# Kernel optimization log

Measured on AMD Instinct MI355X. Metric: run time of the kernel, lower is better.

The kernel has to match this reference:

```python
import jax, jax.numpy as jnp
import numpy as np
from jax import lax

NUM_CHANNELS = 64
DILATION_DEPTH = 9
NUM_REPEAT = 2
KERNEL_SIZE = 3
DILATIONS = [2 ** d for d in range(DILATION_DEPTH)] * NUM_REPEAT  # 18 layers
B, T = 4, 32768


def causal_conv1d(x, w, b, dilation):
    # x: [B, Cin, T], w: [Cout, Cin, K], b: [Cout]
    # left-pad by (K-1)*dilation -> causal, output length T
    pad = (w.shape[-1] - 1) * dilation
    out = lax.conv_general_dilated(
        x, w, window_strides=(1,), padding=[(pad, 0)],
        rhs_dilation=(dilation,), dimension_numbers=("NCH", "OIH", "NCH"))
    return out + b[None, :, None]


def setup_inputs() -> dict:
    key = jax.random.key(0)
    ks = jax.random.split(key, 9)
    L, C = len(DILATIONS), NUM_CHANNELS
    s = 0.05
    return {
        "x": jax.random.normal(ks[0], (B, 1, T), dtype=jnp.float32),
        "in_w": jax.random.normal(ks[1], (C, 1, 1), dtype=jnp.float32) * s,
        "in_b": jax.random.normal(ks[2], (C,), dtype=jnp.float32) * s,
        "hid_w": jax.random.normal(ks[3], (L, 2 * C, C, KERNEL_SIZE), dtype=jnp.float32) * s,
        "hid_b": jax.random.normal(ks[4], (L, 2 * C), dtype=jnp.float32) * s,
        "res_w": jax.random.normal(ks[5], (L, C, C, 1), dtype=jnp.float32) * s,
        "res_b": jax.random.normal(ks[6], (L, C), dtype=jnp.float32) * s,
        "mix_w": jax.random.normal(ks[7], (1, L * C, 1), dtype=jnp.float32) * s,
        "mix_b": jax.random.normal(ks[8], (1,), dtype=jnp.float32) * s,
    }


def reference(x, in_w, in_b, hid_w, hid_b, res_w, res_b, mix_w, mix_b):
    C = NUM_CHANNELS
    out = causal_conv1d(x, in_w, in_b, 1)  # [B, C, T]
    skips = []
    for i, d in enumerate(DILATIONS):
        inp = out
        h = causal_conv1d(inp, hid_w[i], hid_b[i], d)  # [B, 2C, T]
        gated = jnp.tanh(h[:, :C]) * jax.nn.sigmoid(h[:, C:])  # [B, C, T]
        skips.append(gated)
        out = causal_conv1d(gated, res_w[i], res_b[i], 1) + inp
    skip_cat = jnp.concatenate(skips, axis=1)  # [B, L*C, T]
    return causal_conv1d(skip_cat, mix_w, mix_b, 1)  # [B, 1, T]
```

## Files before the change

kernel.cpp:

```cpp
#include <hip/hip_runtime.h>
#include <math.h>

#define T_LEN 32768
#define NB 4
#define NC 64
#define NL 18
#define TILE_T 64

typedef __attribute__((ext_vector_type(8))) short s16x8;
typedef __attribute__((ext_vector_type(4))) float f32x4;
#define MFMA_F16 __builtin_amdgcn_mfma_f32_16x16x32_f16

__device__ inline unsigned short f2h(float f) {
    _Float16 h = (_Float16)f;
    return __builtin_bit_cast(unsigned short, h);
}
__device__ inline unsigned pack_h2(float a, float b) {
    return (unsigned)f2h(a) | ((unsigned)f2h(b) << 16);
}
__device__ inline float h2f(unsigned short u) {
    return (float)__builtin_bit_cast(_Float16, u);
}
__device__ inline float fast_sigmoid(float x) {
    return __builtin_amdgcn_rcpf(1.f + __expf(-x));
}
__device__ inline float fast_tanh(float x) {
    return 1.f - 2.f * __builtin_amdgcn_rcpf(1.f + __expf(2.f * x));
}

__global__ void prep_kernel(const float* __restrict__ hid_w,
                            const float* __restrict__ res_w,
                            const float* __restrict__ mix_b,
                            unsigned short* __restrict__ Wh,
                            unsigned short* __restrict__ Wr,
                            float* __restrict__ out,
                            float* __restrict__ zerobuf) {
    const int nW1 = NL * 128 * 192;
    const int nW2 = NL * 64 * 64;
    const int nOut = NB * T_LEN;
    const int total = nW1 + nW2 + nOut + 32;
    for (int gid = blockIdx.x * blockDim.x + threadIdx.x; gid < total;
         gid += gridDim.x * blockDim.x) {
        if (gid < nW1) {
            int K = gid % 192;
            int co = (gid / 192) & 127;
            int i = gid / (192 * 128);
            int kt = K >> 6, ci = K & 63;
            Wh[gid] = f2h(hid_w[((i * 128 + co) * 64 + ci) * 3 + kt]);
        } else if (gid < nW1 + nW2) {
            int q = gid - nW1;
            int c = q & 63, co = (q >> 6) & 63, i = q >> 12;
            Wr[q] = f2h(res_w[(i * 64 + co) * 64 + c]);
        } else if (gid < nW1 + nW2 + nOut) {
            out[gid - (nW1 + nW2)] = mix_b[0];
        } else {
            zerobuf[gid - (nW1 + nW2 + nOut)] = 0.f;
        }
    }
}

template <int DIL, bool FIRST, bool LAST>
__launch_bounds__(256, 4)
__global__ void layer_kernel(const unsigned short* __restrict__ actH,
                             unsigned short* __restrict__ outH,
                             const unsigned short* __restrict__ Wh,
                             const float* __restrict__ hb,
                             const unsigned short* __restrict__ Wr,
                             const float* __restrict__ rb,
                             const float* __restrict__ mw,
                             float* __restrict__ skip,
                             const float* __restrict__ zerobuf,
                             const float* __restrict__ x,
                             const float* __restrict__ in_w,
                             const float* __restrict__ in_b) {
    constexpr bool UNI = (DIL < 64);
    constexpr int R = UNI ? (64 + 2 * DIL) : 192;
    constexpr int SLOTS = R * 8;
    constexpr int JMAX = (SLOTS + 255) / 256;
    constexpr int GS_BASE = (UNI ? 128 : 0) * 128;
    constexpr int OUT_BASE = (UNI ? 0 : 64) * 128;

    __shared__ uint4 Xs[1536];
    __shared__ float Sk[256];
    char* lds = (char*)Xs;

    const int tid = threadIdx.x;
    const int w = tid >> 6;
    const int l = tid & 63;
    const int lo = l & 15;
    const int hi = l >> 4;
    const int b = blockIdx.y;
    const int tile = (blockIdx.x & 7) * 64 + (blockIdx.x >> 3);
    const int t0 = tile * TILE_T;
    const int m0 = 16 * w;
    const int c0 = m0 + 4 * hi;

    const unsigned short* actB = actH + (size_t)b * T_LEN * NC;
    const float* xB = x + (size_t)b * T_LEN;

    if (FIRST) {
#pragma unroll
        for (int j = 0; j < JMAX; j++) {
            int p = j * 256 + tid;
            if (p < SLOTS) {
                int row = p >> 3, ch = p & 7;
                int tg = t0 + row - 2 * DIL;
                unsigned uu[4] = {0u, 0u, 0u, 0u};
                if (tg >= 0) {
                    float a = xB[tg];
#pragma unroll
                    for (int e = 0; e < 4; e++) {
                        float v0 = a * in_w[ch * 8 + 2 * e] + in_b[ch * 8 + 2 * e];
                        float v1 = a * in_w[ch * 8 + 2 * e + 1] + in_b[ch * 8 + 2 * e + 1];
                        uu[e] = pack_h2(v0, v1);
                    }
                }
                int byte = (row * 128 + ch * 16) ^ ((row & 7) << 4);
                *(uint4*)(lds + byte) = make_uint4(uu[0], uu[1], uu[2], uu[3]);
            }
        }
    } else {
#pragma unroll
        for (int j = 0; j < JMAX; j++) {
            int s = (w * JMAX + j) * 64 + l;
            const void* src;
            if (s >= SLOTS) {
                src = (const void*)(zerobuf + (s & 7) * 4);
            } else {
                int row = s >> 3, ch = s & 7;
                int chunk = ch ^ (row & 7);
                int tg = t0 + (UNI ? (row - 2 * DIL)
                                   : (((row >> 6) - 2) * DIL + (row & 63)));
                src = (tg >= 0) ? (const void*)(actB + (size_t)tg * 64 + chunk * 8)
                                : (const void*)(zerobuf + chunk * 4);
            }
            __builtin_amdgcn_global_load_lds(
                (const __attribute__((address_space(1))) unsigned int*)src,
                (__attribute__((address_space(3))) unsigned int*)(lds +
                                                        (w * JMAX + j) * 1024),
                16, 0, 0);
        }
    }

    s16x8 AH[2][6];
    s16x8 AR[2];
#pragma unroll
    for (int mt = 0; mt < 2; mt++) {
        const unsigned short* wp = Wh + (size_t)(m0 + 64 * mt + lo) * 192;
#pragma unroll
        for (int s = 0; s < 6; s++)
            AH[mt][s] = *(const s16x8*)(wp + 32 * s + 8 * hi);
    }
    if (!LAST) {
#pragma unroll
        for (int s = 0; s < 2; s++)
            AR[s] = *(const s16x8*)(Wr + (size_t)(m0 + lo) * 64 + 32 * s + 8 * hi);
    }

    float bA[4], bB[4], rbv[4];
#pragma unroll
    for (int r = 0; r < 4; r++) {
        bA[r] = hb[c0 + r];
        bB[r] = hb[64 + c0 + r];
        rbv[r] = LAST ? 0.f : rb[c0 + r];
    }
    const float4 mw4 = *(const float4*)(mw + c0);

    __syncthreads();

    f32x4 acc[2][4];
#pragma unroll
    for (int mt = 0; mt < 2; mt++)
#pragma unroll
        for (int nt = 0; nt < 4; nt++)
            acc[mt][nt] = (f32x4){0.f, 0.f, 0.f, 0.f};

#pragma unroll
    for (int s = 0; s < 6; s++) {
        const int tap = s >> 1, half = s & 1;
#pragma unroll
        for (int nt = 0; nt < 4; nt++) {
            int t = 16 * nt + lo;
            int row = UNI ? (t + tap * DIL) : (tap * 64 + t);
            int byte = (row * 128 + half * 64 + hi * 16) ^ ((row & 7) << 4);
            s16x8 bx = __builtin_bit_cast(s16x8, *(const uint4*)(lds + byte));
            acc[0][nt] = MFMA_F16(AH[0][s], bx, acc[0][nt], 0, 0, 0);
            acc[1][nt] = MFMA_F16(AH[1][s], bx, acc[1][nt], 0, 0, 0);
        }
    }

    float4 inp[4];
    if (!LAST) {
#pragma unroll
        for (int nt = 0; nt < 4; nt++) {
            int t = 16 * nt + lo;
            int rowI = UNI ? (t + 2 * DIL) : (128 + t);
            int byteI = (rowI * 128 + c0 * 2) ^ ((rowI & 7) << 4);
            uint2 hv = *(const uint2*)(lds + byteI);
            inp[nt] = make_float4(h2f((unsigned short)(hv.x & 0xffff)),
                                  h2f((unsigned short)(hv.x >> 16)),
                                  h2f((unsigned short)(hv.y & 0xffff)),
                                  h2f((unsigned short)(hv.y >> 16)));
        }
    }

    __syncthreads();

#pragma unroll
    for (int nt = 0; nt < 4; nt++) {
        float g[4];
#pragma unroll
        for (int r = 0; r < 4; r++) {
            float hA = acc[0][nt][r] + bA[r];
            float hB = acc[1][nt][r] + bB[r];
            g[r] = fast_tanh(hA) * fast_sigmoid(hB);
        }
        int t = 16 * nt + lo;
        if (!LAST) {
            int byte = (t * 128 + c0 * 2) ^ ((t & 7) << 4);
            *(uint2*)(lds + GS_BASE + byte) =
                make_uint2(pack_h2(g[0], g[1]), pack_h2(g[2], g[3]));
        }
        float sk = g[0] * mw4.x + g[1] * mw4.y + g[2] * mw4.z + g[3] * mw4.w;
        sk += __shfl_xor(sk, 16, 64);
        sk += __shfl_xor(sk, 32, 64);
        if (hi == 0) Sk[w * 64 + nt * 16 + lo] = sk;
    }
    __syncthreads();

    if (LAST) {
        if (tid < 64) {
            float s2 = Sk[tid] + Sk[64 + tid] + Sk[128 + tid] + Sk[192 + tid];
            skip[(size_t)b * T_LEN + t0 + tid] += s2;
        }
        return;
    }

    f32x4 acc2[4];
#pragma unroll
    for (int nt = 0; nt < 4; nt++) acc2[nt] = (f32x4){0.f, 0.f, 0.f, 0.f};
#pragma unroll
    for (int s = 0; s < 2; s++) {
#pragma unroll
        for (int nt = 0; nt < 4; nt++) {
            int t = 16 * nt + lo;
            int byte = (t * 128 + s * 64 + hi * 16) ^ ((t & 7) << 4);
            s16x8 bg = __builtin_bit_cast(
                s16x8, *(const uint4*)(lds + GS_BASE + byte));
            acc2[nt] = MFMA_F16(AR[s], bg, acc2[nt], 0, 0, 0);
        }
    }

    char* OutH = lds + OUT_BASE;
#pragma unroll
    for (int nt = 0; nt < 4; nt++) {
        int t = 16 * nt + lo;
        float ox = acc2[nt][0] + rbv[0] + inp[nt].x;
        float oy = acc2[nt][1] + rbv[1] + inp[nt].y;
        float oz = acc2[nt][2] + rbv[2] + inp[nt].z;
        float ow = acc2[nt][3] + rbv[3] + inp[nt].w;
        int byteB = (t * 128 + c0 * 2) ^ ((t & 7) << 4);
        *(uint2*)(OutH + byteB) = make_uint2(pack_h2(ox, oy), pack_h2(oz, ow));
    }

    if (tid < 64) {
        float s2 = Sk[tid] + Sk[64 + tid] + Sk[128 + tid] + Sk[192 + tid];
        skip[(size_t)b * T_LEN + t0 + tid] += s2;
    }
    __syncthreads();

    unsigned short* gH = outH + (size_t)b * T_LEN * NC + (size_t)t0 * 64;
#pragma unroll
    for (int i = 0; i < 2; i++) {
        int u = i * 256 + tid;
        int t = u >> 3, ch = u & 7;
        uint4 v = *(const uint4*)(OutH + t * 128 + ((ch ^ (t & 7)) << 4));
        ((uint4*)gH)[u] = v;
    }
}

extern "C" void kernel_launch(void* const* d_in, const int* in_sizes, int n_in,
                              void* d_out, int out_size, void* d_ws, size_t ws_size,
                              hipStream_t stream) {
    const float* x     = (const float*)d_in[0];
    const float* in_w  = (const float*)d_in[1];
    const float* in_b  = (const float*)d_in[2];
    const float* hid_w = (const float*)d_in[3];
    const float* hid_b = (const float*)d_in[4];
    const float* res_w = (const float*)d_in[5];
    const float* res_b = (const float*)d_in[6];
    const float* mix_w = (const float*)d_in[7];
    const float* mix_b = (const float*)d_in[8];
    float* out = (float*)d_out;

    const size_t actN = (size_t)NB * T_LEN * NC;
    unsigned short* H0 = (unsigned short*)d_ws;
    unsigned short* H1 = H0 + actN;
    unsigned short* Wh = H1 + actN;
    unsigned short* Wr = Wh + (size_t)NL * 128 * 192;
    float* zerobuf = (float*)(Wr + (size_t)NL * 64 * 64);

    prep_kernel<<<512, 256, 0, stream>>>(hid_w, res_w, mix_b, Wh, Wr, out,
                                         zerobuf);

    static const int dils[NL] = {1, 2, 4, 8, 16, 32, 64, 128, 256,
                                 1, 2, 4, 8, 16, 32, 64, 128, 256};
    const unsigned short* srcH = H0;
    unsigned short* dstH = H1;
    dim3 grid(T_LEN / TILE_T, NB);

#define LL(D, F, L)                                                           \
    layer_kernel<D, F, L><<<grid, 256, 0, stream>>>(                          \
        srcH, dstH, Wh + (size_t)i * 128 * 192, hid_b + (size_t)i * 128,      \
        Wr + (size_t)i * 64 * 64, res_b + (size_t)i * 64,                     \
        mix_w + (size_t)i * 64, out, zerobuf, x, in_w, in_b)

    for (int i = 0; i < NL; i++) {
        if (i == 0) {
            LL(1, true, false);
        } else if (i == NL - 1) {
            LL(256, false, true);
        } else {
            switch (dils[i]) {
                case 1:   LL(1, false, false);   break;
                case 2:   LL(2, false, false);   break;
                case 4:   LL(4, false, false);   break;
                case 8:   LL(8, false, false);   break;
                case 16:  LL(16, false, false);  break;
                case 32:  LL(32, false, false);  break;
                case 64:  LL(64, false, false);  break;
                case 128: LL(128, false, false); break;
                case 256: LL(256, false, false); break;
            }
        }
        const unsigned short* tH = srcH; srcH = dstH; dstH = (unsigned short*)tH;
    }
#undef LL
}
```

Before: 380.2 us.

## Process two 64-step subtiles per block with double-buffered async LDS loads

Each block now handles 128 time steps as two 64-step subtiles, issuing the global-to-LDS loads for both subtiles up front into separate LDS regions. Barriers wait only on the first subtile's loads (vmcnt(JMAX)), so the second subtile's loads can overlap the first subtile's MFMA and gating work. It also halves the grid and amortizes per-block weight and bias register loads across two subtiles. LDS use doubles per block, which may reduce occupancy, and the custom waitcnt barriers depend on the load-issue order staying as written.

```diff
diff --git a/kernel.cpp b/kernel.cpp
--- a/kernel.cpp
+++ b/kernel.cpp
@@ -5,11 +5,24 @@
 #define NB 4
 #define NC 64
 #define NL 18
-#define TILE_T 64
 
 typedef __attribute__((ext_vector_type(8))) short s16x8;
 typedef __attribute__((ext_vector_type(4))) float f32x4;
 #define MFMA_F16 __builtin_amdgcn_mfma_f32_16x16x32_f16
+
+#define BAR_LGKM()                                                   \
+    do {                                                             \
+        asm volatile("s_waitcnt lgkmcnt(0)" ::: "memory");           \
+        __builtin_amdgcn_s_barrier();                                \
+        __builtin_amdgcn_sched_barrier(0);                           \
+    } while (0)
+#define BAR_VM(N)                                                    \
+    do {                                                             \
+        asm volatile("s_waitcnt vmcnt(%0) lgkmcnt(0)" ::             \
+                         "i"(N) : "memory");                         \
+        __builtin_amdgcn_s_barrier();                                \
+        __builtin_amdgcn_sched_barrier(0);                           \
+    } while (0)
 
 __device__ inline unsigned short f2h(float f) {
     _Float16 h = (_Float16)f;
@@ -79,8 +92,9 @@
     constexpr int JMAX = (SLOTS + 255) / 256;
     constexpr int GS_BASE = (UNI ? 128 : 0) * 128;
     constexpr int OUT_BASE = (UNI ? 0 : 64) * 128;
-
-    __shared__ uint4 Xs[1536];
+    constexpr int REG = 24576;
+
+    __shared__ uint4 Xs[2 * 1536];
     __shared__ float Sk[256];
     char* lds = (char*)Xs;
 
@@ -90,58 +104,14 @@
     const int lo = l & 15;
     const int hi = l >> 4;
     const int b = blockIdx.y;
-    const int tile = (blockIdx.x & 7) * 64 + (blockIdx.x >> 3);
-    const int t0 = tile * TILE_T;
+    const int tile = (blockIdx.x & 7) * 32 + (blockIdx.x >> 3);
+    const int t0 = tile * 128;
     const int m0 = 16 * w;
     const int c0 = m0 + 4 * hi;
 
     const unsigned short* actB = actH + (size_t)b * T_LEN * NC;
     const float* xB = x + (size_t)b * T_LEN;
 
-    if (FIRST) {
-#pragma unroll
-        for (int j = 0; j < JMAX; j++) {
-            int p = j * 256 + tid;
-            if (p < SLOTS) {
-                int row = p >> 3, ch = p & 7;
-                int tg = t0 + row - 2 * DIL;
-                unsigned uu[4] = {0u, 0u, 0u, 0u};
-                if (tg >= 0) {
-                    float a = xB[tg];
-#pragma unroll
-                    for (int e = 0; e < 4; e++) {
-                        float v0 = a * in_w[ch * 8 + 2 * e] + in_b[ch * 8 + 2 * e];
-                        float v1 = a * in_w[ch * 8 + 2 * e + 1] + in_b[ch * 8 + 2 * e + 1];
-                        uu[e] = pack_h2(v0, v1);
-                    }
-                }
-                int byte = (row * 128 + ch * 16) ^ ((row & 7) << 4);
-                *(uint4*)(lds + byte) = make_uint4(uu[0], uu[1], uu[2], uu[3]);
-            }
-        }
-    } else {
-#pragma unroll
-        for (int j = 0; j < JMAX; j++) {
-            int s = (w * JMAX + j) * 64 + l;
-            const void* src;
-            if (s >= SLOTS) {
-                src = (const void*)(zerobuf + (s & 7) * 4);
-            } else {
-                int row = s >> 3, ch = s & 7;
-                int chunk = ch ^ (row & 7);
-                int tg = t0 + (UNI ? (row - 2 * DIL)
-                                   : (((row >> 6) - 2) * DIL + (row & 63)));
-                src = (tg >= 0) ? (const void*)(actB + (size_t)tg * 64 + chunk * 8)
-                                : (const void*)(zerobuf + chunk * 4);
-            }
-            __builtin_amdgcn_global_load_lds(
-                (const __attribute__((address_space(1))) unsigned int*)src,
-                (__attribute__((address_space(3))) unsigned int*)(lds +
-                                                        (w * JMAX + j) * 1024),
-                16, 0, 0);
-        }
-    }
-
     s16x8 AH[2][6];
     s16x8 AR[2];
 #pragma unroll
@@ -156,7 +126,6 @@
         for (int s = 0; s < 2; s++)
             AR[s] = *(const s16x8*)(Wr + (size_t)(m0 + lo) * 64 + 32 * s + 8 * hi);
     }
-
     float bA[4], bB[4], rbv[4];
 #pragma unroll
     for (int r = 0; r < 4; r++) {
@@ -166,116 +135,183 @@
     }
     const float4 mw4 = *(const float4*)(mw + c0);
 
-    __syncthreads();
-
-    f32x4 acc[2][4];
-#pragma unroll
-    for (int mt = 0; mt < 2; mt++)
-#pragma unroll
-        for (int nt = 0; nt < 4; nt++)
-            acc[mt][nt] = (f32x4){0.f, 0.f, 0.f, 0.f};
-
-#pragma unroll
-    for (int s = 0; s < 6; s++) {
-        const int tap = s >> 1, half = s & 1;
+    if (FIRST) {
+#pragma unroll
+        for (int sub = 0; sub < 2; sub++) {
+            char* X = lds + sub * REG;
+            const int tb = t0 + sub * 64;
+#pragma unroll
+            for (int j = 0; j < JMAX; j++) {
+                int p = j * 256 + tid;
+                if (p < SLOTS) {
+                    int row = p >> 3, ch = p & 7;
+                    int tg = tb + row - 2 * DIL;
+                    unsigned uu[4] = {0u, 0u, 0u, 0u};
+                    if (tg >= 0) {
+                        float a = xB[tg];
+#pragma unroll
+                        for (int e = 0; e < 4; e++) {
+                            float v0 = a * in_w[ch * 8 + 2 * e] + in_b[ch * 8 + 2 * e];
+                            float v1 = a * in_w[ch * 8 + 2 * e + 1] + in_b[ch * 8 + 2 * e + 1];
+                            uu[e] = pack_h2(v0, v1);
+                        }
+                    }
+                    int byte = (row * 128 + ch * 16) ^ ((row & 7) << 4);
+                    *(uint4*)(X + byte) = make_uint4(uu[0], uu[1], uu[2], uu[3]);
+                }
+            }
+        }
+    } else {
+#pragma unroll
+        for (int sub = 0; sub < 2; sub++) {
+            char* X = lds + sub * REG;
+            const int tb = t0 + sub * 64;
+#pragma unroll
+            for (int j = 0; j < JMAX; j++) {
+                int s = (w * JMAX + j) * 64 + l;
+                const void* src;
+                if (s >= SLOTS) {
+                    src = (const void*)(zerobuf + (s & 7) * 4);
+                } else {
+                    int row = s >> 3, ch = s & 7;
+                    int chunk = ch ^ (row & 7);
+                    int tg = tb + (UNI ? (row - 2 * DIL)
+                                       : (((row >> 6) - 2) * DIL + (row & 63)));
+                    src = (tg >= 0)
+                              ? (const void*)(actB + (size_t)tg * 64 + chunk * 8)
+                              : (const void*)(zerobuf + chunk * 4);
+                }
+                __builtin_amdgcn_global_load_lds(
+                    (const __attribute__((address_space(1))) unsigned int*)src,
+                    (__attribute__((address_space(3))) unsigned int*)(X +
+                                                        (w * JMAX + j) * 1024),
+                    16, 0, 0);
+            }
+        }
+    }
+
+#pragma unroll
+    for (int sub = 0; sub < 2; sub++) {
+        char* X = lds + sub * REG;
+        const int tt0 = t0 + sub * 64;
+
+        if (FIRST) {
+            BAR_LGKM();
+        } else if (sub == 0) {
+            BAR_VM(JMAX);
+        } else {
+            BAR_VM(0);
+        }
+
+        f32x4 acc[2][4];
+#pragma unroll
+        for (int mt = 0; mt < 2; mt++)
+#pragma unroll
+            for (int nt = 0; nt < 4; nt++)
+                acc[mt][nt] = (f32x4){0.f, 0.f, 0.f, 0.f};
+#pragma unroll
+        for (int s = 0; s < 6; s++) {
+            const int tap = s >> 1, half = s & 1;
+#pragma unroll
+            for (int nt = 0; nt < 4; nt++) {
+                int t = 16 * nt + lo;
+                int row = UNI ? (t + tap * DIL) : (tap * 64 + t);
+                int byte = (row * 128 + half * 64 + hi * 16) ^ ((row & 7) << 4);
+                s16x8 bx = __builtin_bit_cast(s16x8, *(const uint4*)(X + byte));
+                acc[0][nt] = MFMA_F16(AH[0][s], bx, acc[0][nt], 0, 0, 0);
+                acc[1][nt] = MFMA_F16(AH[1][s], bx, acc[1][nt], 0, 0, 0);
+            }
+        }
+
+        float4 inp[4];
+        if (!LAST) {
+#pragma unroll
+            for (int nt = 0; nt < 4; nt++) {
+                int t = 16 * nt + lo;
+                int rowI = UNI ? (t + 2 * DIL) : (128 + t);
+                int byteI = (rowI * 128 + c0 * 2) ^ ((rowI & 7) << 4);
+                uint2 hv = *(const uint2*)(X + byteI);
+                inp[nt] = make_float4(h2f((unsigned short)(hv.x & 0xffff)),
+                                      h2f((unsigned short)(hv.x >> 16)),
+                                      h2f((unsigned short)(hv.y & 0xffff)),
+                                      h2f((unsigned short)(hv.y >> 16)));
+            }
+        }
+
+        BAR_LGKM();
+
+#pragma unroll
+        for (int nt = 0; nt < 4; nt++) {
+            float g[4];
+#pragma unroll
+            for (int r = 0; r < 4; r++) {
+                float hA = acc[0][nt][r] + bA[r];
+                float hB = acc[1][nt][r] + bB[r];
+                g[r] = fast_tanh(hA) * fast_sigmoid(hB);
+            }
+            int t = 16 * nt + lo;
+            if (!LAST) {
+                int byte = (t * 128 + c0 * 2) ^ ((t & 7) << 4);
+                *(uint2*)(X + GS_BASE + byte) =
+                    make_uint2(pack_h2(g[0], g[1]), pack_h2(g[2], g[3]));
+            }
+            float sk = g[0] * mw4.x + g[1] * mw4.y + g[2] * mw4.z + g[3] * mw4.w;
+            sk += __shfl_xor(sk, 16, 64);
+            sk += __shfl_xor(sk, 32, 64);
+            if (hi == 0) Sk[w * 64 + nt * 16 + lo] = sk;
+        }
+        BAR_LGKM();
+
+        if (LAST) {
+            if (tid < 64) {
+                float s2 = Sk[tid] + Sk[64 + tid] + Sk[128 + tid] + Sk[192 + tid];
+                skip[(size_t)b * T_LEN + tt0 + tid] += s2;
+            }
+            continue;
+        }
+
+        f32x4 acc2[4];
+#pragma unroll
+        for (int nt = 0; nt < 4; nt++) acc2[nt] = (f32x4){0.f, 0.f, 0.f, 0.f};
+#pragma unroll
+        for (int s = 0; s < 2; s++) {
+#pragma unroll
+            for (int nt = 0; nt < 4; nt++) {
+                int t = 16 * nt + lo;
+                int byte = (t * 128 + s * 64 + hi * 16) ^ ((t & 7) << 4);
+                s16x8 bg = __builtin_bit_cast(
+                    s16x8, *(const uint4*)(X + GS_BASE + byte));
+                acc2[nt] = MFMA_F16(AR[s], bg, acc2[nt], 0, 0, 0);
+            }
+        }
+
+        char* OutH = X + OUT_BASE;
 #pragma unroll
         for (int nt = 0; nt < 4; nt++) {
             int t = 16 * nt + lo;
-            int row = UNI ? (t + tap * DIL) : (tap * 64 + t);
-            int byte = (row * 128 + half * 64 + hi * 16) ^ ((row & 7) << 4);
-            s16x8 bx = __builtin_bit_cast(s16x8, *(const uint4*)(lds + byte));
-            acc[0][nt] = MFMA_F16(AH[0][s], bx, acc[0][nt], 0, 0, 0);
-            acc[1][nt] = MFMA_F16(AH[1][s], bx, acc[1][nt], 0, 0, 0);
-        }
-    }
-
-    float4 inp[4];
-    if (!LAST) {
-#pragma unroll
-        for (int nt = 0; nt < 4; nt++) {
-            int t = 16 * nt + lo;
-            int rowI = UNI ? (t + 2 * DIL) : (128 + t);
-            int byteI = (rowI * 128 + c0 * 2) ^ ((rowI & 7) << 4);
-            uint2 hv = *(const uint2*)(lds + byteI);
-            inp[nt] = make_float4(h2f((unsigned short)(hv.x & 0xffff)),
-                                  h2f((unsigned short)(hv.x >> 16)),
-                                  h2f((unsigned short)(hv.y & 0xffff)),
-                                  h2f((unsigned short)(hv.y >> 16)));
-        }
-    }
-
-    __syncthreads();
-
-#pragma unroll
-    for (int nt = 0; nt < 4; nt++) {
-        float g[4];
-#pragma unroll
-        for (int r = 0; r < 4; r++) {
-            float hA = acc[0][nt][r] + bA[r];
-            float hB = acc[1][nt][r] + bB[r];
-            g[r] = fast_tanh(hA) * fast_sigmoid(hB);
-        }
-        int t = 16 * nt + lo;
-        if (!LAST) {
-            int byte = (t * 128 + c0 * 2) ^ ((t & 7) << 4);
-            *(uint2*)(lds + GS_BASE + byte) =
-                make_uint2(pack_h2(g[0], g[1]), pack_h2(g[2], g[3]));
-        }
-        float sk = g[0] * mw4.x + g[1] * mw4.y + g[2] * mw4.z + g[3] * mw4.w;
-        sk += __shfl_xor(sk, 16, 64);
-        sk += __shfl_xor(sk, 32, 64);
-        if (hi == 0) Sk[w * 64 + nt * 16 + lo] = sk;
-    }
-    __syncthreads();
-
-    if (LAST) {
+            float ox = acc2[nt][0] + rbv[0] + inp[nt].x;
+            float oy = acc2[nt][1] + rbv[1] + inp[nt].y;
+            float oz = acc2[nt][2] + rbv[2] + inp[nt].z;
+            float ow = acc2[nt][3] + rbv[3] + inp[nt].w;
+            int byteB = (t * 128 + c0 * 2) ^ ((t & 7) << 4);
+            *(uint2*)(OutH + byteB) =
+                make_uint2(pack_h2(ox, oy), pack_h2(oz, ow));
+        }
+
         if (tid < 64) {
             float s2 = Sk[tid] + Sk[64 + tid] + Sk[128 + tid] + Sk[192 + tid];
-            skip[(size_t)b * T_LEN + t0 + tid] += s2;
-        }
-        return;
-    }
-
-    f32x4 acc2[4];
-#pragma unroll
-    for (int nt = 0; nt < 4; nt++) acc2[nt] = (f32x4){0.f, 0.f, 0.f, 0.f};
-#pragma unroll
-    for (int s = 0; s < 2; s++) {
-#pragma unroll
-        for (int nt = 0; nt < 4; nt++) {
-            int t = 16 * nt + lo;
-            int byte = (t * 128 + s * 64 + hi * 16) ^ ((t & 7) << 4);
-            s16x8 bg = __builtin_bit_cast(
-                s16x8, *(const uint4*)(lds + GS_BASE + byte));
-            acc2[nt] = MFMA_F16(AR[s], bg, acc2[nt], 0, 0, 0);
-        }
-    }
-
-    char* OutH = lds + OUT_BASE;
-#pragma unroll
-    for (int nt = 0; nt < 4; nt++) {
-        int t = 16 * nt + lo;
-        float ox = acc2[nt][0] + rbv[0] + inp[nt].x;
-        float oy = acc2[nt][1] + rbv[1] + inp[nt].y;
-        float oz = acc2[nt][2] + rbv[2] + inp[nt].z;
-        float ow = acc2[nt][3] + rbv[3] + inp[nt].w;
-        int byteB = (t * 128 + c0 * 2) ^ ((t & 7) << 4);
-        *(uint2*)(OutH + byteB) = make_uint2(pack_h2(ox, oy), pack_h2(oz, ow));
-    }
-
-    if (tid < 64) {
-        float s2 = Sk[tid] + Sk[64 + tid] + Sk[128 + tid] + Sk[192 + tid];
-        skip[(size_t)b * T_LEN + t0 + tid] += s2;
-    }
-    __syncthreads();
-
-    unsigned short* gH = outH + (size_t)b * T_LEN * NC + (size_t)t0 * 64;
-#pragma unroll
-    for (int i = 0; i < 2; i++) {
-        int u = i * 256 + tid;
-        int t = u >> 3, ch = u & 7;
-        uint4 v = *(const uint4*)(OutH + t * 128 + ((ch ^ (t & 7)) << 4));
-        ((uint4*)gH)[u] = v;
+            skip[(size_t)b * T_LEN + tt0 + tid] += s2;
+        }
+        BAR_LGKM();
+
+        unsigned short* gH = outH + (size_t)b * T_LEN * NC + (size_t)tt0 * 64;
+#pragma unroll
+        for (int i = 0; i < 2; i++) {
+            int u = i * 256 + tid;
+            int t = u >> 3, ch = u & 7;
+            uint4 v = *(const uint4*)(OutH + t * 128 + ((ch ^ (t & 7)) << 4));
+            ((uint4*)gH)[u] = v;
+        }
     }
 }
 
@@ -307,7 +343,7 @@
                                  1, 2, 4, 8, 16, 32, 64, 128, 256};
     const unsigned short* srcH = H0;
     unsigned short* dstH = H1;
-    dim3 grid(T_LEN / TILE_T, NB);
+    dim3 grid(T_LEN / 128, NB);
 
 #define LL(D, F, L)                                                           \
     layer_kernel<D, F, L><<<grid, 256, 0, stream>>>(                          \
```

New measurement: 373.9 us. About the same (-1.7%).
